# Performance work log

Measured on AMD Instinct MI355X. Metric: run time of the kernel, lower is better.

The kernel has to match this reference:

```python
import jax, jax.numpy as jnp
import numpy as np
import math

B, S, DM, H = 2, 2048, 1024, 16
HD = DM // H  # head_dim = 64


def setup_inputs() -> dict:
    key = jax.random.key(0)
    ks = jax.random.split(key, 7)
    mk = lambda k, shp, s=1.0: jax.random.normal(k, shp, dtype=jnp.float32) * s
    return {
        "q": mk(ks[0], (B, S, DM)),
        "k": mk(ks[1], (B, S, DM)),
        "v": mk(ks[2], (B, S, DM)),
        "wq": mk(ks[3], (DM, DM), 0.02),
        "wk": mk(ks[4], (DM, DM), 0.02),
        "wv": mk(ks[5], (DM, DM), 0.02),
        "wo": mk(ks[6], (DM, DM), 0.02),
    }


def reference(q, k, v, wq, wk, wv, wo):
    bsz, seqlen, _ = q.shape
    # bias-free linear projections: y = x @ W.T (torch nn.Linear layout [out,in])
    def proj(x, w):
        y = jnp.einsum('bsd,ed->bse', x, w)
        return y.reshape(bsz, seqlen, H, HD).transpose(0, 2, 1, 3)  # (B,H,S,HD)
    xq, xk, xv = proj(q, wq), proj(k, wk), proj(v, wv)
    scores = jnp.einsum('bhqd,bhkd->bhqk', xq, xk) / math.sqrt(HD)  # (B,H,S,S)
    # causal mask: -inf above the diagonal
    causal = jnp.tril(jnp.ones((seqlen, seqlen), dtype=bool))
    scores = jnp.where(causal[None, None], scores, -jnp.inf)
    probs = jax.nn.softmax(scores.astype(jnp.float32), axis=-1).astype(xq.dtype)
    # dropout p=0.0 -> identity in eval / p=0 config
    out = jnp.einsum('bhqk,bhkd->bhqd', probs, xv)  # (B,H,S,HD)
    out = out.transpose(0, 2, 1, 3).reshape(bsz, seqlen, DM)
    return jnp.einsum('bsd,ed->bse', out, wo)
```

## Files before the change

kernel.cpp:

```cpp
#include <hip/hip_runtime.h>
#include <hip/hip_bf16.h>
#include <stdint.h>

#define NB 2
#define NS 2048
#define NDM 1024
#define NH 16
#define NHD 64
#define NTOK (NB * NS)

typedef __bf16 bf16x8 __attribute__((ext_vector_type(8)));
typedef float f32x4 __attribute__((ext_vector_type(4)));
typedef uint16_t u16x8 __attribute__((ext_vector_type(8)));

static __device__ __forceinline__ uint16_t f2bf(float f) {
  __bf16 b = (__bf16)f;
  union { __bf16 b; uint16_t u; } x; x.b = b;
  return x.u;
}

static __device__ __forceinline__ u16x8 cvt8(float4 a, float4 b) {
  u16x8 v;
  v[0] = f2bf(a.x); v[1] = f2bf(a.y); v[2] = f2bf(a.z); v[3] = f2bf(a.w);
  v[4] = f2bf(b.x); v[5] = f2bf(b.y); v[6] = f2bf(b.z); v[7] = f2bf(b.w);
  return v;
}

static __device__ __forceinline__ void gload_lds16(const void* g, void* l) {
  __builtin_amdgcn_global_load_lds(
      (const __attribute__((address_space(1))) void*)g,
      (__attribute__((address_space(3))) void*)l, 16, 0, 0);
}

__global__ __launch_bounds__(256) void cvt_w(
    const float* __restrict__ w0, const float* __restrict__ w1,
    const float* __restrict__ w2, const float* __restrict__ w3,
    uint16_t* __restrict__ o0, uint16_t* __restrict__ o1,
    uint16_t* __restrict__ o2, uint16_t* __restrict__ o3) {
  int y = blockIdx.y;
  const float* src = (y == 0) ? w0 : (y == 1) ? w1 : (y == 2) ? w2 : w3;
  uint16_t* dst = (y == 0) ? o0 : (y == 1) ? o1 : (y == 2) ? o2 : o3;
  int i = ((int)blockIdx.x * 256 + (int)threadIdx.x) * 8;
  float4 a = *(const float4*)(src + i);
  float4 b = *(const float4*)(src + i + 4);
  *(u16x8*)&dst[i] = cvt8(a, b);
}

__global__ __launch_bounds__(256) void proj_gemm(
    const float* __restrict__ q, const float* __restrict__ k,
    const float* __restrict__ v, const uint16_t* __restrict__ wqb,
    const uint16_t* __restrict__ wkb, const uint16_t* __restrict__ wvb,
    uint16_t* __restrict__ XQ, uint16_t* __restrict__ XK,
    uint16_t* __restrict__ XVT) {
  __shared__ uint16_t As[128][72];
  __shared__ uint16_t Bs[128][64];
  int z = blockIdx.z;
  const float* A = (z == 0) ? q : (z == 1) ? k : v;
  const uint16_t* W = (z == 0) ? wqb : (z == 1) ? wkb : wvb;
  int m0 = blockIdx.x * 128, n0 = blockIdx.y * 128;
  int tid = threadIdx.x;
  int lane = tid & 63, w = tid >> 6;
  int g = lane >> 4, r16 = lane & 15;
  int wm = w >> 1, wn = w & 1;
  int bce = ((lane & 7) ^ ((lane >> 3) & 7)) * 8;
  int brlane = lane >> 3;

  f32x4 acc[4][4] = {};
  float4 a0[4], a1[4];

  #pragma unroll
  for (int cc = 0; cc < 4; ++cc) {
    int ch = tid + cc * 256;
    int row = ch >> 3, c8 = ch & 7;
    const float* src = A + (size_t)(m0 + row) * NDM + c8 * 8;
    a0[cc] = *(const float4*)src;
    a1[cc] = *(const float4*)(src + 4);
  }

  for (int k0 = 0; k0 < NDM; k0 += 64) {
    __syncthreads();
    #pragma unroll
    for (int cc = 0; cc < 4; ++cc) {
      int ch = tid + cc * 256;
      int row = ch >> 3, c8 = ch & 7;
      *(u16x8*)&As[row][c8 * 8] = cvt8(a0[cc], a1[cc]);
    }
    #pragma unroll
    for (int i = 0; i < 4; ++i) {
      int brow = w * 32 + i * 8;
      const uint16_t* src =
          W + (size_t)(n0 + brow + brlane) * NDM + k0 + bce;
      gload_lds16(src, &Bs[brow][0]);
    }
    __syncthreads();

    if (k0 + 64 < NDM) {
      #pragma unroll
      for (int cc = 0; cc < 4; ++cc) {
        int ch = tid + cc * 256;
        int row = ch >> 3, c8 = ch & 7;
        const float* src = A + (size_t)(m0 + row) * NDM + (k0 + 64) + c8 * 8;
        a0[cc] = *(const float4*)src;
        a1[cc] = *(const float4*)(src + 4);
      }
    }

    #pragma unroll
    for (int kc = 0; kc < 2; ++kc) {
      bf16x8 af[4], bf[4];
      #pragma unroll
      for (int i = 0; i < 4; ++i) {
        af[i] = *(const bf16x8*)&As[wm * 64 + i * 16 + r16][kc * 32 + g * 8];
        int gran = (kc * 4 + g) ^ (r16 & 7);
        bf[i] = *(const bf16x8*)&Bs[wn * 64 + i * 16 + r16][gran * 8];
      }
      #pragma unroll
      for (int mi = 0; mi < 4; ++mi)
        #pragma unroll
        for (int ni = 0; ni < 4; ++ni)
          acc[mi][ni] = __builtin_amdgcn_mfma_f32_16x16x32_bf16(
              af[mi], bf[ni], acc[mi][ni], 0, 0, 0);
    }
  }

  float scale = (z == 0) ? 0.125f * 1.44269504088896340736f : 1.0f;
  #pragma unroll
  for (int mi = 0; mi < 4; ++mi) {
    #pragma unroll
    for (int ni = 0; ni < 4; ++ni) {
      int m = m0 + wm * 64 + mi * 16 + g * 4;
      int n = n0 + wn * 64 + ni * 16 + r16;
      f32x4 a = acc[mi][ni];
      if (z == 2) {
        ushort4 pk;
        pk.x = f2bf(a[0]); pk.y = f2bf(a[1]);
        pk.z = f2bf(a[2]); pk.w = f2bf(a[3]);
        *(ushort4*)&XVT[(size_t)n * NTOK + m] = pk;
      } else {
        uint16_t* Y = (z == 0) ? XQ : XK;
        #pragma unroll
        for (int j = 0; j < 4; ++j)
          Y[(size_t)(m + j) * NDM + n] = f2bf(a[j] * scale);
      }
    }
  }
}

__global__ __launch_bounds__(256) void attn_kernel(
    const uint16_t* __restrict__ XQ, const uint16_t* __restrict__ XK,
    const uint16_t* __restrict__ XVT, uint16_t* __restrict__ AO) {
  __shared__ uint16_t Klds[64][72];
  __shared__ uint16_t Vlds[64][72];
  __shared__ uint16_t Plds[4][16][72];

  int tid = threadIdx.x;
  int lane = tid & 63;
  int w = tid >> 6;
  int g = lane >> 4, r16 = lane & 15;
  int srow = tid >> 2;
  int scol = (tid & 3) * 16;

  int item = (int)blockIdx.x;
  int qc = 31 - (item >> 5);
  int bh = item & 31;
  int b = bh >> 4, h = bh & 15;
  int q0 = qc * 64;
  int q0w = q0 + w * 16;
  int T = qc + 1;

  const uint16_t* qb =
      XQ + (size_t)(b * NS + q0w + r16) * NDM + h * NHD + g * 8;
  bf16x8 qf0 = *(const bf16x8*)qb;
  bf16x8 qf1 = *(const bf16x8*)(qb + 32);

  f32x4 oacc[4] = {};
  float mrow = -1e30f, lsum = 0.f;

  const uint16_t* kbase = XK + (size_t)(b * NS + srow) * NDM + h * NHD + scol;
  const uint16_t* vbase = XVT + (size_t)(h * NHD + srow) * NTOK + b * NS + scol;

  u16x8 kr0 = *(const u16x8*)(kbase);
  u16x8 kr1 = *(const u16x8*)(kbase + 8);
  u16x8 vr0 = *(const u16x8*)(vbase);
  u16x8 vr1 = *(const u16x8*)(vbase + 8);

  for (int t = 0; t < T; ++t) {
    int kv0 = t * 64;
    __syncthreads();
    *(u16x8*)&Klds[srow][scol]     = kr0;
    *(u16x8*)&Klds[srow][scol + 8] = kr1;
    *(u16x8*)&Vlds[srow][scol]     = vr0;
    *(u16x8*)&Vlds[srow][scol + 8] = vr1;
    __syncthreads();
    if (t + 1 < T) {
      const uint16_t* kp = kbase + (size_t)(t + 1) * 64 * NDM;
      const uint16_t* vp = vbase + (t + 1) * 64;
      kr0 = *(const u16x8*)(kp);
      kr1 = *(const u16x8*)(kp + 8);
      vr0 = *(const u16x8*)(vp);
      vr1 = *(const u16x8*)(vp + 8);
    }

    f32x4 sc[4];
    __builtin_amdgcn_s_setprio(1);
    #pragma unroll
    for (int t4 = 0; t4 < 4; ++t4) {
      bf16x8 kf0 = *(const bf16x8*)&Klds[t4 * 16 + r16][g * 8];
      bf16x8 kf1 = *(const bf16x8*)&Klds[t4 * 16 + r16][32 + g * 8];
      f32x4 x = __builtin_amdgcn_mfma_f32_16x16x32_bf16(
          kf0, qf0, (f32x4){0.f, 0.f, 0.f, 0.f}, 0, 0, 0);
      x = __builtin_amdgcn_mfma_f32_16x16x32_bf16(kf1, qf1, x, 0, 0, 0);
      sc[t4] = x;
    }
    __builtin_amdgcn_s_setprio(0);

    #pragma unroll
    for (int t4 = 0; t4 < 4; ++t4) {
      if (kv0 + t4 * 16 + 15 > q0w) {
        #pragma unroll
        for (int j = 0; j < 4; ++j)
          if (kv0 + t4 * 16 + g * 4 + j > q0w + r16) sc[t4][j] = -1e30f;
      }
    }

    float m16 = fmaxf(
        fmaxf(fmaxf(fmaxf(sc[0][0], sc[0][1]), fmaxf(sc[0][2], sc[0][3])),
              fmaxf(fmaxf(sc[1][0], sc[1][1]), fmaxf(sc[1][2], sc[1][3]))),
        fmaxf(fmaxf(fmaxf(sc[2][0], sc[2][1]), fmaxf(sc[2][2], sc[2][3])),
              fmaxf(fmaxf(sc[3][0], sc[3][1]), fmaxf(sc[3][2], sc[3][3]))));
    m16 = fmaxf(m16, __shfl_xor(m16, 16));
    m16 = fmaxf(m16, __shfl_xor(m16, 32));

    if (!__all(m16 <= mrow + 8.0f)) {
      float mnew = fmaxf(mrow, m16);
      float sf = __builtin_amdgcn_exp2f(mrow - mnew);
      mrow = mnew;
      lsum *= sf;
      #pragma unroll
      for (int j = 0; j < 4; ++j) {
        float sfj = __shfl(sf, g * 4 + j);
        #pragma unroll
        for (int dt = 0; dt < 4; ++dt) oacc[dt][j] *= sfj;
      }
    }

    #pragma unroll
    for (int t4 = 0; t4 < 4; ++t4) {
      float p0 = __builtin_amdgcn_exp2f(sc[t4][0] - mrow);
      float p1 = __builtin_amdgcn_exp2f(sc[t4][1] - mrow);
      float p2 = __builtin_amdgcn_exp2f(sc[t4][2] - mrow);
      float p3 = __builtin_amdgcn_exp2f(sc[t4][3] - mrow);
      lsum += (p0 + p1) + (p2 + p3);
      ushort4 pk;
      pk.x = f2bf(p0); pk.y = f2bf(p1); pk.z = f2bf(p2); pk.w = f2bf(p3);
      *(ushort4*)&Plds[w][r16][t4 * 16 + g * 4] = pk;
    }

    bf16x8 pa0 = *(const bf16x8*)&Plds[w][r16][g * 8];
    bf16x8 pa1 = *(const bf16x8*)&Plds[w][r16][32 + g * 8];
    __builtin_amdgcn_s_setprio(1);
    #pragma unroll
    for (int dt = 0; dt < 4; ++dt) {
      bf16x8 vf0 = *(const bf16x8*)&Vlds[dt * 16 + r16][g * 8];
      bf16x8 vf1 = *(const bf16x8*)&Vlds[dt * 16 + r16][32 + g * 8];
      oacc[dt] = __builtin_amdgcn_mfma_f32_16x16x32_bf16(pa0, vf0, oacc[dt], 0, 0, 0);
      oacc[dt] = __builtin_amdgcn_mfma_f32_16x16x32_bf16(pa1, vf1, oacc[dt], 0, 0, 0);
    }
    __builtin_amdgcn_s_setprio(0);
  }

  float l2 = lsum + __shfl_xor(lsum, 16);
  float ltot = l2 + __shfl_xor(l2, 32);
  #pragma unroll
  for (int j = 0; j < 4; ++j) {
    float lt = __shfl(ltot, g * 4 + j);
    float inv = 1.0f / lt;
    size_t ro = (size_t)(b * NS + q0 + w * 16 + g * 4 + j) * NDM + h * NHD;
    #pragma unroll
    for (int dt = 0; dt < 4; ++dt)
      AO[ro + dt * 16 + r16] = f2bf(oacc[dt][j] * inv);
  }
}

__global__ __launch_bounds__(256) void out_gemm(
    const uint16_t* __restrict__ AO, const uint16_t* __restrict__ wob,
    float* __restrict__ out) {
  __shared__ uint16_t As[128][64];
  __shared__ uint16_t Bs[128][64];
  int m0 = blockIdx.x * 128, n0 = blockIdx.y * 128;
  int tid = threadIdx.x;
  int lane = tid & 63, w = tid >> 6;
  int g = lane >> 4, r16 = lane & 15;
  int wm = w >> 1, wn = w & 1;
  int bce = ((lane & 7) ^ ((lane >> 3) & 7)) * 8;
  int brlane = lane >> 3;

  f32x4 acc[4][4] = {};

  for (int k0 = 0; k0 < NDM; k0 += 64) {
    __syncthreads();
    #pragma unroll
    for (int i = 0; i < 4; ++i) {
      int row = w * 32 + i * 8;
      const uint16_t* asrc =
          AO + (size_t)(m0 + row + brlane) * NDM + k0 + bce;
      gload_lds16(asrc, &As[row][0]);
      const uint16_t* bsrc =
          wob + (size_t)(n0 + row + brlane) * NDM + k0 + bce;
      gload_lds16(bsrc, &Bs[row][0]);
    }
    __syncthreads();

    #pragma unroll
    for (int kc = 0; kc < 2; ++kc) {
      bf16x8 af[4], bf[4];
      #pragma unroll
      for (int i = 0; i < 4; ++i) {
        int gran = (kc * 4 + g) ^ (r16 & 7);
        af[i] = *(const bf16x8*)&As[wm * 64 + i * 16 + r16][gran * 8];
        bf[i] = *(const bf16x8*)&Bs[wn * 64 + i * 16 + r16][gran * 8];
      }
      #pragma unroll
      for (int mi = 0; mi < 4; ++mi)
        #pragma unroll
        for (int ni = 0; ni < 4; ++ni)
          acc[mi][ni] = __builtin_amdgcn_mfma_f32_16x16x32_bf16(
              af[mi], bf[ni], acc[mi][ni], 0, 0, 0);
    }
  }

  #pragma unroll
  for (int mi = 0; mi < 4; ++mi) {
    #pragma unroll
    for (int ni = 0; ni < 4; ++ni) {
      int m = m0 + wm * 64 + mi * 16 + g * 4;
      int n = n0 + wn * 64 + ni * 16 + r16;
      #pragma unroll
      for (int j = 0; j < 4; ++j)
        out[(size_t)(m + j) * NDM + n] = acc[mi][ni][j];
    }
  }
}

extern "C" void kernel_launch(void* const* d_in, const int* in_sizes, int n_in,
                              void* d_out, int out_size, void* d_ws,
                              size_t ws_size, hipStream_t stream) {
  const float* q  = (const float*)d_in[0];
  const float* k  = (const float*)d_in[1];
  const float* v  = (const float*)d_in[2];
  const float* wq = (const float*)d_in[3];
  const float* wk = (const float*)d_in[4];
  const float* wv = (const float*)d_in[5];
  const float* wo = (const float*)d_in[6];

  uint16_t* XQ  = (uint16_t*)d_ws;
  uint16_t* XK  = XQ + (size_t)NTOK * NDM;
  uint16_t* XVT = XK + (size_t)NTOK * NDM;
  uint16_t* AO  = XVT + (size_t)NTOK * NDM;
  uint16_t* WQB = AO + (size_t)NTOK * NDM;
  uint16_t* WKB = WQB + (size_t)NDM * NDM;
  uint16_t* WVB = WKB + (size_t)NDM * NDM;
  uint16_t* WOB = WVB + (size_t)NDM * NDM;

  cvt_w<<<dim3(NDM * NDM / (256 * 8), 4), 256, 0, stream>>>(
      wq, wk, wv, wo, WQB, WKB, WVB, WOB);
  proj_gemm<<<dim3(NTOK / 128, NDM / 128, 3), 256, 0, stream>>>(
      q, k, v, WQB, WKB, WVB, XQ, XK, XVT);
  attn_kernel<<<dim3(1024), 256, 0, stream>>>(XQ, XK, XVT, AO);
  out_gemm<<<dim3(NTOK / 128, NDM / 128), 256, 0, stream>>>(
      AO, WOB, (float*)d_out);
}
```

Baseline: 125.7 us.

## Double-buffer LDS tiles in projection and output GEMMs

Both the QKV projection GEMM and the output GEMM now keep two LDS stages for A and B. The next k-tile is issued into the other buffer while MFMAs run on the current one, so each iteration needs one barrier instead of two. The projection GEMM also swaps its padded A tile for an XOR-swizzled layout that matches B's reads, to avoid LDS bank conflicts. The price is twice the shared memory per block, which may reduce occupancy, and the fp32 A prefetch now runs two tiles ahead, which raises register pressure.

New measurement: 120.1 us. -4.4%, faster.

```diff
diff --git a/kernel.cpp b/kernel.cpp
--- a/kernel.cpp
+++ b/kernel.cpp
@@ -52,8 +52,8 @@
     const uint16_t* __restrict__ wkb, const uint16_t* __restrict__ wvb,
     uint16_t* __restrict__ XQ, uint16_t* __restrict__ XK,
     uint16_t* __restrict__ XVT) {
-  __shared__ uint16_t As[128][72];
-  __shared__ uint16_t Bs[128][64];
+  __shared__ uint16_t As[2][128][64];
+  __shared__ uint16_t Bs[2][128][64];
   int z = blockIdx.z;
   const float* A = (z == 0) ? q : (z == 1) ? k : v;
   const uint16_t* W = (z == 0) ? wqb : (z == 1) ? wkb : wvb;
@@ -76,32 +76,53 @@
     a0[cc] = *(const float4*)src;
     a1[cc] = *(const float4*)(src + 4);
   }
-
-  for (int k0 = 0; k0 < NDM; k0 += 64) {
-    __syncthreads();
-    #pragma unroll
-    for (int cc = 0; cc < 4; ++cc) {
-      int ch = tid + cc * 256;
-      int row = ch >> 3, c8 = ch & 7;
-      *(u16x8*)&As[row][c8 * 8] = cvt8(a0[cc], a1[cc]);
-    }
-    #pragma unroll
-    for (int i = 0; i < 4; ++i) {
-      int brow = w * 32 + i * 8;
-      const uint16_t* src =
-          W + (size_t)(n0 + brow + brlane) * NDM + k0 + bce;
-      gload_lds16(src, &Bs[brow][0]);
-    }
-    __syncthreads();
-
-    if (k0 + 64 < NDM) {
+  #pragma unroll
+  for (int i = 0; i < 4; ++i) {
+    int brow = w * 32 + i * 8;
+    gload_lds16(W + (size_t)(n0 + brow + brlane) * NDM + bce, &Bs[0][brow][0]);
+  }
+  #pragma unroll
+  for (int cc = 0; cc < 4; ++cc) {
+    int ch = tid + cc * 256;
+    int row = ch >> 3, c8 = ch & 7;
+    *(u16x8*)&As[0][row][((c8 ^ (row & 7)) * 8)] = cvt8(a0[cc], a1[cc]);
+  }
+  #pragma unroll
+  for (int cc = 0; cc < 4; ++cc) {
+    int ch = tid + cc * 256;
+    int row = ch >> 3, c8 = ch & 7;
+    const float* src = A + (size_t)(m0 + row) * NDM + 64 + c8 * 8;
+    a0[cc] = *(const float4*)src;
+    a1[cc] = *(const float4*)(src + 4);
+  }
+  __syncthreads();
+
+  for (int t = 0; t < 16; ++t) {
+    int cur = t & 1, nxt = cur ^ 1;
+    if (t < 15) {
+      int k1 = (t + 1) * 64;
+      #pragma unroll
+      for (int i = 0; i < 4; ++i) {
+        int brow = w * 32 + i * 8;
+        gload_lds16(W + (size_t)(n0 + brow + brlane) * NDM + k1 + bce,
+                    &Bs[nxt][brow][0]);
+      }
       #pragma unroll
       for (int cc = 0; cc < 4; ++cc) {
         int ch = tid + cc * 256;
         int row = ch >> 3, c8 = ch & 7;
-        const float* src = A + (size_t)(m0 + row) * NDM + (k0 + 64) + c8 * 8;
-        a0[cc] = *(const float4*)src;
-        a1[cc] = *(const float4*)(src + 4);
+        *(u16x8*)&As[nxt][row][((c8 ^ (row & 7)) * 8)] = cvt8(a0[cc], a1[cc]);
+      }
+      if (t < 14) {
+        int k2 = (t + 2) * 64;
+        #pragma unroll
+        for (int cc = 0; cc < 4; ++cc) {
+          int ch = tid + cc * 256;
+          int row = ch >> 3, c8 = ch & 7;
+          const float* src = A + (size_t)(m0 + row) * NDM + k2 + c8 * 8;
+          a0[cc] = *(const float4*)src;
+          a1[cc] = *(const float4*)(src + 4);
+        }
       }
     }
 
@@ -110,9 +131,9 @@
       bf16x8 af[4], bf[4];
       #pragma unroll
       for (int i = 0; i < 4; ++i) {
-        af[i] = *(const bf16x8*)&As[wm * 64 + i * 16 + r16][kc * 32 + g * 8];
         int gran = (kc * 4 + g) ^ (r16 & 7);
-        bf[i] = *(const bf16x8*)&Bs[wn * 64 + i * 16 + r16][gran * 8];
+        af[i] = *(const bf16x8*)&As[cur][wm * 64 + i * 16 + r16][gran * 8];
+        bf[i] = *(const bf16x8*)&Bs[cur][wn * 64 + i * 16 + r16][gran * 8];
       }
       #pragma unroll
       for (int mi = 0; mi < 4; ++mi)
@@ -121,6 +142,7 @@
           acc[mi][ni] = __builtin_amdgcn_mfma_f32_16x16x32_bf16(
               af[mi], bf[ni], acc[mi][ni], 0, 0, 0);
     }
+    __syncthreads();
   }
 
   float scale = (z == 0) ? 0.125f * 1.44269504088896340736f : 1.0f;
@@ -285,8 +307,8 @@
 __global__ __launch_bounds__(256) void out_gemm(
     const uint16_t* __restrict__ AO, const uint16_t* __restrict__ wob,
     float* __restrict__ out) {
-  __shared__ uint16_t As[128][64];
-  __shared__ uint16_t Bs[128][64];
+  __shared__ uint16_t As[2][128][64];
+  __shared__ uint16_t Bs[2][128][64];
   int m0 = blockIdx.x * 128, n0 = blockIdx.y * 128;
   int tid = threadIdx.x;
   int lane = tid & 63, w = tid >> 6;
@@ -297,19 +319,27 @@
 
   f32x4 acc[4][4] = {};
 
-  for (int k0 = 0; k0 < NDM; k0 += 64) {
-    __syncthreads();
-    #pragma unroll
-    for (int i = 0; i < 4; ++i) {
-      int row = w * 32 + i * 8;
-      const uint16_t* asrc =
-          AO + (size_t)(m0 + row + brlane) * NDM + k0 + bce;
-      gload_lds16(asrc, &As[row][0]);
-      const uint16_t* bsrc =
-          wob + (size_t)(n0 + row + brlane) * NDM + k0 + bce;
-      gload_lds16(bsrc, &Bs[row][0]);
-    }
-    __syncthreads();
+  #pragma unroll
+  for (int i = 0; i < 4; ++i) {
+    int row = w * 32 + i * 8;
+    gload_lds16(AO + (size_t)(m0 + row + brlane) * NDM + bce, &As[0][row][0]);
+    gload_lds16(wob + (size_t)(n0 + row + brlane) * NDM + bce, &Bs[0][row][0]);
+  }
+  __syncthreads();
+
+  for (int t = 0; t < 16; ++t) {
+    int cur = t & 1, nxt = cur ^ 1;
+    if (t < 15) {
+      int k1 = (t + 1) * 64;
+      #pragma unroll
+      for (int i = 0; i < 4; ++i) {
+        int row = w * 32 + i * 8;
+        gload_lds16(AO + (size_t)(m0 + row + brlane) * NDM + k1 + bce,
+                    &As[nxt][row][0]);
+        gload_lds16(wob + (size_t)(n0 + row + brlane) * NDM + k1 + bce,
+                    &Bs[nxt][row][0]);
+      }
+    }
 
     #pragma unroll
     for (int kc = 0; kc < 2; ++kc) {
@@ -317,8 +347,8 @@
       #pragma unroll
       for (int i = 0; i < 4; ++i) {
         int gran = (kc * 4 + g) ^ (r16 & 7);
-        af[i] = *(const bf16x8*)&As[wm * 64 + i * 16 + r16][gran * 8];
-        bf[i] = *(const bf16x8*)&Bs[wn * 64 + i * 16 + r16][gran * 8];
+        af[i] = *(const bf16x8*)&As[cur][wm * 64 + i * 16 + r16][gran * 8];
+        bf[i] = *(const bf16x8*)&Bs[cur][wn * 64 + i * 16 + r16][gran * 8];
       }
       #pragma unroll
       for (int mi = 0; mi < 4; ++mi)
@@ -327,6 +357,7 @@
           acc[mi][ni] = __builtin_amdgcn_mfma_f32_16x16x32_bf16(
               af[mi], bf[ni], acc[mi][ni], 0, 0, 0);
     }
+    __syncthreads();
   }
 
   #pragma unroll
```
